# Kernel optimization log

Hardware: AMD Instinct MI355X
Metric: run time of the kernel (lower is better)

Reference implementation:

```python
import jax, jax.numpy as jnp
import numpy as np

N, E, G = 10000, 100000, 64
NB, EMB, S, COUT, LMAX = 16, 16, 8, 16, 2
RMAX = 4.0
WNUM = (LMAX + 1) * COUT * S * S  # 3072 per-edge TP weights


def setup_inputs() -> dict:
    key = jax.random.key(0)
    ks = jax.random.split(key, 16)
    def lin(k, i, o):
        return (jax.random.normal(k, (i, o), jnp.float32) / np.sqrt(i)).astype(jnp.float32)
    return {
        "pos": jax.random.normal(ks[0], (N, 3), jnp.float32),
        "A": jax.random.randint(ks[1], (N,), 0, 10),
        "batch": jnp.sort(jax.random.randint(ks[2], (N,), 0, G)),
        "edge_src": jax.random.randint(ks[3], (E,), 0, N),
        "edge_dst": jax.random.randint(ks[4], (E,), 0, N),
        "edge_shifts": jnp.zeros((E, 3), jnp.float32),
        "cell": jax.random.normal(ks[5], (G, 3, 3), jnp.float32),
        "emb_table": jax.random.normal(ks[6], (10, EMB), jnp.float32),
        "mlp_w1": lin(ks[7], EMB, 64), "mlp_b1": jnp.zeros((64,), jnp.float32),
        "mlp_w2": lin(ks[8], 64, S), "mlp_b2": jnp.zeros((S,), jnp.float32),
        "fc_w1": lin(ks[9], NB, 64), "fc_b1": jnp.zeros((64,), jnp.float32),
        "fc_w2": lin(ks[10], 64, 64), "fc_b2": jnp.zeros((64,), jnp.float32),
        "fc_w3": lin(ks[11], 64, WNUM), "fc_b3": jnp.zeros((WNUM,), jnp.float32),
    }


def _forward(pos, edge_shifts, cell, emb_table, mlp_w1, mlp_b1, mlp_w2, mlp_b2,
             fc_w1, fc_b1, fc_w2, fc_b2, fc_w3, fc_b3, A, batch, edge_src, edge_dst):
    # periodic-image edge vectors: shifts @ cell[graph of src node]
    shift = jnp.einsum('ei,eij->ej', edge_shifts, cell[batch[edge_src]])
    vec = pos[edge_dst] - pos[edge_src] + shift                     # (E,3)
    r = jnp.linalg.norm(vec, axis=1)                                # (E,)
    n = vec / jnp.maximum(r, 1e-9)[:, None]                         # unit edge direction
    # per-node scalar features: atom_mlp(atom_embedding(A))
    Ai = jax.nn.silu(emb_table[A] @ mlp_w1 + mlp_b1) @ mlp_w2 + mlp_b2  # (N,S)
    # radial basis: gaussian soft-one-hot on [0, RMAX] with cutoff, * sqrt(NB)
    vals = jnp.linspace(0.0, RMAX, NB + 2)[1:-1]
    step = RMAX / (NB + 1)
    emb = jnp.exp(-(((r[:, None] - vals) / step) ** 2)) / 1.12 * np.sqrt(NB)  # (E,NB)
    # radial MLP -> per-edge tensor-product weights
    h = jax.nn.silu(emb @ fc_w1 + fc_b1)
    h = jax.nn.silu(h @ fc_w2 + fc_b2)
    W = (h @ fc_w3 + fc_b3).reshape(E, LMAX + 1, COUT, S, S)        # (E,L,Cout,C1,C2)
    # f_in rank-L block is Ai[src] x n^{(x)L}; x2 is scalar Ai[dst].
    # The Cartesian TP factorizes: channel mixing once, then attach n^{(x)L}.
    fs, fd = Ai[edge_src], Ai[edge_dst]                             # (E,S)
    m = jnp.einsum('eloab,ea,eb->elo', W, fs, fd)                   # (E,L,Cout)
    out0 = m[:, 0]                                                  # (E,Cout)       rank 0
    out1 = m[:, 1, :, None] * n[:, None, :]                         # (E,Cout,3)     rank 1
    n2 = n[:, :, None] * n[:, None, :]                              # (E,3,3)
    out2 = m[:, 2, :, None, None] * n2[:, None]                     # (E,Cout,3,3)   rank 2
    ef = jnp.concatenate([out0, out1.reshape(E, -1), out2.reshape(E, -1)], axis=-1)  # (E, 13*Cout)
    # scatter-sum to destination nodes, normalize by neighbor count (clamped to 1)
    cnt = jnp.maximum(jax.ops.segment_sum(jnp.ones((E,), ef.dtype), edge_dst, num_segments=N), 1.0)
    return jax.ops.segment_sum(ef, edge_dst, num_segments=N) / cnt[:, None]  # (N, 208)


def reference(pos, A, batch, edge_src, edge_dst, edge_shifts, cell, emb_table,
              mlp_w1, mlp_b1, mlp_w2, mlp_b2, fc_w1, fc_b1, fc_w2, fc_b2, fc_w3, fc_b3):
    return _forward(pos, edge_shifts, cell, emb_table, mlp_w1, mlp_b1, mlp_w2, mlp_b2,
                    fc_w1, fc_b1, fc_w2, fc_b2, fc_w3, fc_b3, A, batch, edge_src, edge_dst)
```

## Files before the change

kernel.cpp:

```cpp
#include <hip/hip_runtime.h>
#include <math.h>
#include <stdint.h>


typedef float  f32x4  __attribute__((ext_vector_type(4)));
typedef short  s16x8  __attribute__((ext_vector_type(8)));
typedef __bf16 bf16x8 __attribute__((ext_vector_type(8)));

__device__ __forceinline__ float silu_f(float x) {
    return x / (1.0f + __expf(-x));
}

__device__ __forceinline__ void split8(f32x4 a, f32x4 b, s16x8& hi, s16x8& lo) {
    bf16x8 h8, l8;
    #pragma unroll
    for (int i = 0; i < 4; ++i) {
        float z = a[i]; __bf16 zh = (__bf16)z; h8[i] = zh; l8[i] = (__bf16)(z - (float)zh);
        float y = b[i]; __bf16 yh = (__bf16)y; h8[4 + i] = yh; l8[4 + i] = (__bf16)(y - (float)yh);
    }
    hi = __builtin_bit_cast(s16x8, h8);
    lo = __builtin_bit_cast(s16x8, l8);
}

__global__ __launch_bounds__(256) void k_setup(const float* __restrict__ w3,
                                               const float* __restrict__ b3,
                                               ushort* __restrict__ wz,
                                               const int* __restrict__ A,
                                               const float* __restrict__ embt,
                                               const float* __restrict__ w1,
                                               const float* __restrict__ b1,
                                               const float* __restrict__ w2,
                                               const float* __restrict__ b2,
                                               float* __restrict__ Ai,
                                               const int* __restrict__ edst,
                                               int* __restrict__ deg,
                                               int N, int E, int aiB) {
    const int b = blockIdx.x;
    const int tid = threadIdx.x;
    if (b < 780) {
        int t = b * 256 + tid;
        int j    = t & 7;
        int l    = (t >> 3) & 63;
        int rest = t >> 9;
        int tt   = rest % 3;
        int s    = rest / 3;
        int lo   = tt * 16 + (l & 15);
        int kl   = (l >> 4) * 8 + j;
        float v;
        if (s < 128) {
            int ab = s >> 1;
            int c  = (s & 1) * 32 + kl;
            v = w3[c * 3072 + lo * 64 + ab];
        } else {
            int ab = (s - 128) * 32 + kl;
            v = b3[lo * 64 + ab];
        }
        __bf16 hi  = (__bf16)v;
        __bf16 lor = (__bf16)(v - (float)hi);
        size_t base = (size_t)(s * 3 + tt) * 2 * 512 + l * 8 + j;
        wz[base]       = __builtin_bit_cast(ushort, hi);
        wz[base + 512] = __builtin_bit_cast(ushort, lor);
    } else if (b < 780 + aiB) {
        int i = (b - 780) * 256 + tid;
        if (i >= N) return;
        float e[16];
        const float* er = embt + A[i] * 16;
        #pragma unroll
        for (int k = 0; k < 16; ++k) e[k] = er[k];
        float h1[64];
        #pragma unroll
        for (int j = 0; j < 64; ++j) {
            float a = b1[j];
            #pragma unroll
            for (int k = 0; k < 16; ++k) a = fmaf(e[k], w1[k * 64 + j], a);
            h1[j] = silu_f(a);
        }
        #pragma unroll
        for (int o = 0; o < 8; ++o) {
            float a = b2[o];
            #pragma unroll
            for (int j = 0; j < 64; ++j) a = fmaf(h1[j], w2[j * 8 + o], a);
            Ai[i * 8 + o] = a;
        }
    } else {
        int e = (b - 780 - aiB) * 256 + tid;
        if (e < E) atomicAdd(&deg[edst[e]], 1);
    }
}

__global__ __launch_bounds__(1024) void k_scan(const int* __restrict__ deg,
                                               int* __restrict__ offs,
                                               int* __restrict__ cursor, int N) {
    __shared__ int part[1024];
    const int t = threadIdx.x;
    const int chunk = (N + 1023) / 1024;
    const int beg = t * chunk;
    const int end = min(beg + chunk, N);
    int s = 0;
    for (int i = beg; i < end; ++i) s += deg[i];
    part[t] = s;
    __syncthreads();
    for (int off = 1; off < 1024; off <<= 1) {
        int v = (t >= off) ? part[t - off] : 0;
        __syncthreads();
        part[t] += v;
        __syncthreads();
    }
    int run = (t == 0) ? 0 : part[t - 1];
    for (int i = beg; i < end; ++i) {
        offs[i] = run;
        cursor[i] = run;
        run += deg[i];
    }
    if (t == 1023) offs[N] = part[1023];
}

__global__ __launch_bounds__(256, 2) void k_edge(
    const float* __restrict__ pos, const int* __restrict__ batch,
    const int* __restrict__ esrc, const int* __restrict__ edst,
    const float* __restrict__ eshift, const float* __restrict__ cell,
    const float* __restrict__ fw1, const float* __restrict__ fb1,
    const float* __restrict__ fw2, const float* __restrict__ fb2,
    const ushort* __restrict__ wz,
    const float* __restrict__ Ai, float* __restrict__ ef,
    int* __restrict__ cursor, int* __restrict__ eidx, int E) {

    __shared__ __align__(16) float s_un[8704];
    __shared__ __align__(16) float s_o[8704];

    const int tid  = threadIdx.x;
    const int lane = tid & 63;
    const int w    = __builtin_amdgcn_readfirstlane(tid >> 6);
    const int e0   = blockIdx.x * 128;
    const int j0   = w * 16;

    const f32x4* wzv = reinterpret_cast<const f32x4*>(wz);
    f32x4 r0 = wzv[w * 192 + lane];
    f32x4 r1 = wzv[w * 192 + 64 + lane];
    f32x4 r2 = wzv[w * 192 + 128 + lane];

    #pragma unroll
    for (int rr = 0; rr < 2; ++rr) {
        const int e = e0 + rr * 64 + lane;
        const bool valid = (e < E);
        const int ec = valid ? e : (E - 1);
        const int src = esrc[ec];
        const int dst = edst[ec];

        const int g0 = batch[src];
        const float s0 = eshift[ec * 3 + 0], s1 = eshift[ec * 3 + 1], s2 = eshift[ec * 3 + 2];
        const float* cl = cell + g0 * 9;
        float vx = pos[dst * 3 + 0] - pos[src * 3 + 0] + s0 * cl[0] + s1 * cl[3] + s2 * cl[6];
        float vy = pos[dst * 3 + 1] - pos[src * 3 + 1] + s0 * cl[1] + s1 * cl[4] + s2 * cl[7];
        float vz = pos[dst * 3 + 2] - pos[src * 3 + 2] + s0 * cl[2] + s1 * cl[5] + s2 * cl[8];
        float r = sqrtf(vx * vx + vy * vy + vz * vz);
        float rinv = 1.0f / fmaxf(r, 1e-9f);
        float nx = vx * rinv, ny = vy * rinv, nz = vz * rinv;

        float embv[16];
        const float step = 4.0f / 17.0f;
        const float sc = 4.0f / 1.12f;
        #pragma unroll
        for (int k = 0; k < 16; ++k) {
            float d = (r - (float)(k + 1) * step) / step;
            embv[k] = __expf(-d * d) * sc;
        }

        const int hb = (rr * 64 + lane) * 65;
        #pragma unroll
        for (int jj = 0; jj < 16; ++jj) {
            const int j = j0 + jj;
            float a = fb1[j];
            #pragma unroll
            for (int k = 0; k < 16; ++k) a = fmaf(embv[k], fw1[k * 64 + j], a);
            s_un[hb + j] = silu_f(a);
        }

        {
            const float* As = Ai + (size_t)src * 8;
            const float* Ad = Ai + (size_t)dst * 8;
            float fsa0 = As[2 * w], fsa1 = As[2 * w + 1];
            f32x4 d0 = *reinterpret_cast<const f32x4*>(Ad);
            f32x4 d1 = *reinterpret_cast<const f32x4*>(Ad + 4);
            float fdv[8] = {d0[0], d0[1], d0[2], d0[3], d1[0], d1[1], d1[2], d1[3]};
            const int ob = (rr * 64 + lane) * 68 + j0;
            #pragma unroll
            for (int i = 0; i < 8; ++i)  s_o[ob + i]     = fsa0 * fdv[i];
            #pragma unroll
            for (int i = 0; i < 8; ++i)  s_o[ob + 8 + i] = fsa1 * fdv[i];
        }

        if (w == 0 && valid) {
            float* np = ef + (size_t)e * 52;
            np[48] = nx; np[49] = ny; np[50] = nz;
            int pp = atomicAdd(&cursor[dst], 1);
            eidx[pp] = e;
        }
    }
    __syncthreads();

    float hcr[2][16];
    #pragma unroll
    for (int rr = 0; rr < 2; ++rr) {
        const int hb = (rr * 64 + lane) * 65;
        #pragma unroll
        for (int i = 0; i < 16; ++i) hcr[rr][i] = fb2[j0 + i];
        #pragma unroll 4
        for (int j = 0; j < 64; ++j) {
            const float v = s_un[hb + j];
            const float* w2r = fw2 + j * 64 + j0;
            #pragma unroll
            for (int i = 0; i < 16; ++i) hcr[rr][i] = fmaf(v, w2r[i], hcr[rr][i]);
        }
        #pragma unroll
        for (int i = 0; i < 16; ++i) hcr[rr][i] = silu_f(hcr[rr][i]);
    }
    __syncthreads();

    #pragma unroll
    for (int rr = 0; rr < 2; ++rr) {
        const int hb = (rr * 64 + lane) * 68 + j0;
        #pragma unroll
        for (int i = 0; i < 16; ++i) s_un[hb + i] = hcr[rr][i];
    }
    __syncthreads();

    const int g = lane >> 4;
    const int mrow = w * 32 + (lane & 15);
    s16x8 AhF[2][2], AlF[2][2], OhF[2][2], OlF[2][2];
    #pragma unroll
    for (int mt = 0; mt < 2; ++mt) {
        const float* hr = s_un + (mrow + mt * 16) * 68;
        const float* orw = s_o + (mrow + mt * 16) * 68;
        f32x4 a0 = *reinterpret_cast<const f32x4*>(hr + g * 8);
        f32x4 a1 = *reinterpret_cast<const f32x4*>(hr + g * 8 + 4);
        split8(a0, a1, AhF[mt][0], AlF[mt][0]);
        f32x4 a2 = *reinterpret_cast<const f32x4*>(hr + 32 + g * 8);
        f32x4 a3 = *reinterpret_cast<const f32x4*>(hr + 32 + g * 8 + 4);
        split8(a2, a3, AhF[mt][1], AlF[mt][1]);
        f32x4 o0 = *reinterpret_cast<const f32x4*>(orw + g * 8);
        f32x4 o1 = *reinterpret_cast<const f32x4*>(orw + g * 8 + 4);
        split8(o0, o1, OhF[mt][0], OlF[mt][0]);
        f32x4 o2 = *reinterpret_cast<const f32x4*>(orw + 32 + g * 8);
        f32x4 o3 = *reinterpret_cast<const f32x4*>(orw + 32 + g * 8 + 4);
        split8(o2, o3, OhF[mt][1], OlF[mt][1]);
    }
    __syncthreads();

    ushort* sBb = reinterpret_cast<ushort*>(s_un);
    const int rb = w * 32 + (lane >> 4) * 4;

    f32x4 acc[2][3];
    #pragma unroll
    for (int mt = 0; mt < 2; ++mt)
        #pragma unroll
        for (int t = 0; t < 3; ++t) acc[mt][t] = (f32x4){0.f, 0.f, 0.f, 0.f};

    for (int u = 0; u < 65; ++u) {
        const int bs = u & 1;
        f32x4* db = reinterpret_cast<f32x4*>(sBb + bs * 6144 + w * 1536);
        db[lane]       = r0;
        db[64 + lane]  = r1;
        db[128 + lane] = r2;
        __syncthreads();
        if (u < 64) {
            const f32x4* gs = wzv + (size_t)(u + 1) * 768 + w * 192;
            r0 = gs[lane];
            r1 = gs[64 + lane];
            r2 = gs[128 + lane];
        }
        const ushort* bbuf = sBb + bs * 6144;
        if (u < 64) {
            float ov[8];
            #pragma unroll
            for (int i = 0; i < 4; ++i) {
                ov[i]     = s_o[(rb + i) * 68 + u];
                ov[4 + i] = s_o[(rb + 16 + i) * 68 + u];
            }
            #pragma unroll
            for (int t = 0; t < 3; ++t) {
                f32x4 D0 = {0.f, 0.f, 0.f, 0.f};
                f32x4 D1 = {0.f, 0.f, 0.f, 0.f};
                #pragma unroll
                for (int sl = 0; sl < 2; ++sl) {
                    const int fo = ((sl * 3 + t) * 2) * 512 + lane * 8;
                    s16x8 Bh = *reinterpret_cast<const s16x8*>(bbuf + fo);
                    s16x8 Bl = *reinterpret_cast<const s16x8*>(bbuf + fo + 512);
                    D0 = __builtin_amdgcn_mfma_f32_16x16x32_bf16(AhF[0][sl], Bh, D0, 0, 0, 0);
                    D0 = __builtin_amdgcn_mfma_f32_16x16x32_bf16(AhF[0][sl], Bl, D0, 0, 0, 0);
                    D0 = __builtin_amdgcn_mfma_f32_16x16x32_bf16(AlF[0][sl], Bh, D0, 0, 0, 0);
                    D1 = __builtin_amdgcn_mfma_f32_16x16x32_bf16(AhF[1][sl], Bh, D1, 0, 0, 0);
                    D1 = __builtin_amdgcn_mfma_f32_16x16x32_bf16(AhF[1][sl], Bl, D1, 0, 0, 0);
                    D1 = __builtin_amdgcn_mfma_f32_16x16x32_bf16(AlF[1][sl], Bh, D1, 0, 0, 0);
                }
                #pragma unroll
                for (int i = 0; i < 4; ++i) {
                    acc[0][t][i] = fmaf(ov[i],     D0[i], acc[0][t][i]);
                    acc[1][t][i] = fmaf(ov[4 + i], D1[i], acc[1][t][i]);
                }
            }
        } else {
            #pragma unroll
            for (int t = 0; t < 3; ++t) {
                #pragma unroll
                for (int sl = 0; sl < 2; ++sl) {
                    const int fo = ((sl * 3 + t) * 2) * 512 + lane * 8;
                    s16x8 Bh = *reinterpret_cast<const s16x8*>(bbuf + fo);
                    s16x8 Bl = *reinterpret_cast<const s16x8*>(bbuf + fo + 512);
                    acc[0][t] = __builtin_amdgcn_mfma_f32_16x16x32_bf16(OhF[0][sl], Bh, acc[0][t], 0, 0, 0);
                    acc[0][t] = __builtin_amdgcn_mfma_f32_16x16x32_bf16(OhF[0][sl], Bl, acc[0][t], 0, 0, 0);
                    acc[0][t] = __builtin_amdgcn_mfma_f32_16x16x32_bf16(OlF[0][sl], Bh, acc[0][t], 0, 0, 0);
                    acc[1][t] = __builtin_amdgcn_mfma_f32_16x16x32_bf16(OhF[1][sl], Bh, acc[1][t], 0, 0, 0);
                    acc[1][t] = __builtin_amdgcn_mfma_f32_16x16x32_bf16(OhF[1][sl], Bl, acc[1][t], 0, 0, 0);
                    acc[1][t] = __builtin_amdgcn_mfma_f32_16x16x32_bf16(OlF[1][sl], Bh, acc[1][t], 0, 0, 0);
                }
            }
        }
    }

    #pragma unroll
    for (int mt = 0; mt < 2; ++mt) {
        #pragma unroll
        for (int t = 0; t < 3; ++t) {
            #pragma unroll
            for (int i = 0; i < 4; ++i) {
                const int ee = e0 + rb + mt * 16 + i;
                if (ee < E) ef[(size_t)ee * 52 + t * 16 + (lane & 15)] = acc[mt][t][i];
            }
        }
    }
}

__global__ __launch_bounds__(256) void k_gather(const float* __restrict__ ef,
                                                const int* __restrict__ offs,
                                                const int* __restrict__ eidx,
                                                float* __restrict__ out, int N) {
    const int lane = threadIdx.x & 63;
    const int node = blockIdx.x * 4 + (threadIdx.x >> 6);
    if (node >= N) return;

    const int beg = offs[node];
    const int end = offs[node + 1];

    int mi[4], ii[4], jj[4], mode[4];
    #pragma unroll
    for (int t = 0; t < 4; ++t) {
        int c = lane + 64 * t;
        if (c < 16)       { mi[t] = c;                 ii[t] = 0;     jj[t] = 0;     mode[t] = 0; }
        else if (c < 64)  { int u = c - 16; mi[t] = 16 + u / 3; ii[t] = u % 3; jj[t] = 0; mode[t] = 1; }
        else if (c < 208) { int u = c - 64; mi[t] = 32 + u / 9; int rr = u % 9; ii[t] = rr / 3; jj[t] = rr % 3; mode[t] = 2; }
        else              { mi[t] = 0; ii[t] = 0; jj[t] = 0; mode[t] = 3; }
    }

    float acc[4] = {0.f, 0.f, 0.f, 0.f};
    for (int k = beg; k < end; ++k) {
        const int e = eidx[k];
        const float* b = ef + (size_t)e * 52;
        float v = (lane < 51) ? b[lane] : 0.0f;
        float n0 = __shfl(v, 48);
        float n1 = __shfl(v, 49);
        float n2 = __shfl(v, 50);
        #pragma unroll
        for (int t = 0; t < 4; ++t) {
            float mval = __shfl(v, mi[t]);
            float ni = (ii[t] == 0) ? n0 : ((ii[t] == 1) ? n1 : n2);
            float nj = (jj[t] == 0) ? n0 : ((jj[t] == 1) ? n1 : n2);
            float f  = (mode[t] == 0) ? 1.0f
                     : (mode[t] == 1) ? ni
                     : (mode[t] == 2) ? ni * nj
                     : 0.0f;
            acc[t] = fmaf(mval, f, acc[t]);
        }
    }

    const float inv = 1.0f / fmaxf((float)(end - beg), 1.0f);
    float* op = out + (size_t)node * 208;
    op[lane]        = acc[0] * inv;
    op[lane + 64]   = acc[1] * inv;
    op[lane + 128]  = acc[2] * inv;
    if (lane < 16) op[lane + 192] = acc[3] * inv;
}

extern "C" void kernel_launch(void* const* d_in, const int* in_sizes, int n_in,
                              void* d_out, int out_size, void* d_ws, size_t ws_size,
                              hipStream_t stream) {
    const float* pos    = (const float*)d_in[0];
    const int*   A      = (const int*)d_in[1];
    const int*   batch  = (const int*)d_in[2];
    const int*   esrc   = (const int*)d_in[3];
    const int*   edst   = (const int*)d_in[4];
    const float* eshift = (const float*)d_in[5];
    const float* cell   = (const float*)d_in[6];
    const float* embt   = (const float*)d_in[7];
    const float* mw1    = (const float*)d_in[8];
    const float* mb1    = (const float*)d_in[9];
    const float* mw2    = (const float*)d_in[10];
    const float* mb2    = (const float*)d_in[11];
    const float* fw1    = (const float*)d_in[12];
    const float* fb1    = (const float*)d_in[13];
    const float* fw2    = (const float*)d_in[14];
    const float* fb2    = (const float*)d_in[15];
    const float* w3     = (const float*)d_in[16];
    const float* b3     = (const float*)d_in[17];
    float* out = (float*)d_out;

    const int N = in_sizes[1];
    const int E = in_sizes[3];

    char* p = (char*)d_ws;
    auto take = [&](size_t bytes) {
        char* q = p;
        p += (bytes + 255) & ~(size_t)255;
        return q;
    };
    ushort* wz    = (ushort*)take((size_t)130 * 3 * 2 * 512 * sizeof(ushort));
    float* Ai     = (float*)take((size_t)N * 8 * sizeof(float));
    int*   deg    = (int*)  take((size_t)N * sizeof(int));
    int*   offs   = (int*)  take((size_t)(N + 1) * sizeof(int));
    int*   cursor = (int*)  take((size_t)N * sizeof(int));
    int*   eidx   = (int*)  take((size_t)E * sizeof(int));
    float* ef     = (float*)take((size_t)E * 52 * sizeof(float));

    hipMemsetAsync(deg, 0, (size_t)N * sizeof(int), stream);

    const int aiB = (N + 255) / 256;
    const int histB = (E + 255) / 256;
    k_setup<<<780 + aiB + histB, 256, 0, stream>>>(w3, b3, wz, A, embt, mw1, mb1,
                                                   mw2, mb2, Ai, edst, deg, N, E, aiB);
    k_scan<<<1, 1024, 0, stream>>>(deg, offs, cursor, N);
    k_edge<<<(E + 127) / 128, 256, 0, stream>>>(pos, batch, esrc, edst, eshift, cell,
                                                fw1, fb1, fw2, fb2, wz, Ai,
                                                ef, cursor, eidx, E);
    k_gather<<<(N + 3) / 4, 256, 0, stream>>>(ef, offs, eidx, out, N);
}
```

Measured before the change: 248.2 us.

## Load TP weight fragments directly into registers, dropping LDS staging and barriers

The per-step B-matrix weight fragments are now loaded from global memory straight into a double-buffered register array, replacing the shared-memory staging buffer and the per-iteration __syncthreads. The loop is unrolled by two so it alternates register buffers, prefetching step u+1 while computing step u. The final o-weighted term runs first, and s_setprio is raised around the MFMA groups. Each wave now loads all 12 fragments itself instead of splitting the load across four waves, which raises VGPR pressure and global/L2 traffic and may lower occupancy.

```diff
diff --git a/kernel.cpp b/kernel.cpp
--- a/kernel.cpp
+++ b/kernel.cpp
@@ -135,9 +135,14 @@
     const int j0   = w * 16;
 
     const f32x4* wzv = reinterpret_cast<const f32x4*>(wz);
-    f32x4 r0 = wzv[w * 192 + lane];
-    f32x4 r1 = wzv[w * 192 + 64 + lane];
-    f32x4 r2 = wzv[w * 192 + 128 + lane];
+
+    s16x8 Ba[12], Bb[12];
+#define LOADB(ARR, U) { \
+    const f32x4* gs = wzv + (size_t)(U) * 768 + lane; \
+    _Pragma("unroll") \
+    for (int f = 0; f < 12; ++f) ARR[f] = __builtin_bit_cast(s16x8, gs[f * 64]); }
+
+    LOADB(Ba, 0);
 
     #pragma unroll
     for (int rr = 0; rr < 2; ++rr) {
@@ -224,6 +229,8 @@
         for (int i = 0; i < 16; ++i) s_un[hb + i] = hcr[rr][i];
     }
     __syncthreads();
+
+    LOADB(Bb, 64);
 
     const int g = lane >> 4;
     const int mrow = w * 32 + (lane & 15);
@@ -245,9 +252,7 @@
         f32x4 o3 = *reinterpret_cast<const f32x4*>(orw + 32 + g * 8 + 4);
         split8(o2, o3, OhF[mt][1], OlF[mt][1]);
     }
-    __syncthreads();
-
-    ushort* sBb = reinterpret_cast<ushort*>(s_un);
+
     const int rb = w * 32 + (lane >> 4) * 4;
 
     f32x4 acc[2][3];
@@ -256,67 +261,64 @@
         #pragma unroll
         for (int t = 0; t < 3; ++t) acc[mt][t] = (f32x4){0.f, 0.f, 0.f, 0.f};
 
-    for (int u = 0; u < 65; ++u) {
-        const int bs = u & 1;
-        f32x4* db = reinterpret_cast<f32x4*>(sBb + bs * 6144 + w * 1536);
-        db[lane]       = r0;
-        db[64 + lane]  = r1;
-        db[128 + lane] = r2;
-        __syncthreads();
-        if (u < 64) {
-            const f32x4* gs = wzv + (size_t)(u + 1) * 768 + w * 192;
-            r0 = gs[lane];
-            r1 = gs[64 + lane];
-            r2 = gs[128 + lane];
-        }
-        const ushort* bbuf = sBb + bs * 6144;
-        if (u < 64) {
-            float ov[8];
-            #pragma unroll
-            for (int i = 0; i < 4; ++i) {
-                ov[i]     = s_o[(rb + i) * 68 + u];
-                ov[4 + i] = s_o[(rb + 16 + i) * 68 + u];
-            }
-            #pragma unroll
-            for (int t = 0; t < 3; ++t) {
-                f32x4 D0 = {0.f, 0.f, 0.f, 0.f};
-                f32x4 D1 = {0.f, 0.f, 0.f, 0.f};
-                #pragma unroll
-                for (int sl = 0; sl < 2; ++sl) {
-                    const int fo = ((sl * 3 + t) * 2) * 512 + lane * 8;
-                    s16x8 Bh = *reinterpret_cast<const s16x8*>(bbuf + fo);
-                    s16x8 Bl = *reinterpret_cast<const s16x8*>(bbuf + fo + 512);
-                    D0 = __builtin_amdgcn_mfma_f32_16x16x32_bf16(AhF[0][sl], Bh, D0, 0, 0, 0);
-                    D0 = __builtin_amdgcn_mfma_f32_16x16x32_bf16(AhF[0][sl], Bl, D0, 0, 0, 0);
-                    D0 = __builtin_amdgcn_mfma_f32_16x16x32_bf16(AlF[0][sl], Bh, D0, 0, 0, 0);
-                    D1 = __builtin_amdgcn_mfma_f32_16x16x32_bf16(AhF[1][sl], Bh, D1, 0, 0, 0);
-                    D1 = __builtin_amdgcn_mfma_f32_16x16x32_bf16(AhF[1][sl], Bl, D1, 0, 0, 0);
-                    D1 = __builtin_amdgcn_mfma_f32_16x16x32_bf16(AlF[1][sl], Bh, D1, 0, 0, 0);
-                }
-                #pragma unroll
-                for (int i = 0; i < 4; ++i) {
-                    acc[0][t][i] = fmaf(ov[i],     D0[i], acc[0][t][i]);
-                    acc[1][t][i] = fmaf(ov[4 + i], D1[i], acc[1][t][i]);
-                }
-            }
-        } else {
-            #pragma unroll
-            for (int t = 0; t < 3; ++t) {
-                #pragma unroll
-                for (int sl = 0; sl < 2; ++sl) {
-                    const int fo = ((sl * 3 + t) * 2) * 512 + lane * 8;
-                    s16x8 Bh = *reinterpret_cast<const s16x8*>(bbuf + fo);
-                    s16x8 Bl = *reinterpret_cast<const s16x8*>(bbuf + fo + 512);
-                    acc[0][t] = __builtin_amdgcn_mfma_f32_16x16x32_bf16(OhF[0][sl], Bh, acc[0][t], 0, 0, 0);
-                    acc[0][t] = __builtin_amdgcn_mfma_f32_16x16x32_bf16(OhF[0][sl], Bl, acc[0][t], 0, 0, 0);
-                    acc[0][t] = __builtin_amdgcn_mfma_f32_16x16x32_bf16(OlF[0][sl], Bh, acc[0][t], 0, 0, 0);
-                    acc[1][t] = __builtin_amdgcn_mfma_f32_16x16x32_bf16(OhF[1][sl], Bh, acc[1][t], 0, 0, 0);
-                    acc[1][t] = __builtin_amdgcn_mfma_f32_16x16x32_bf16(OhF[1][sl], Bl, acc[1][t], 0, 0, 0);
-                    acc[1][t] = __builtin_amdgcn_mfma_f32_16x16x32_bf16(OlF[1][sl], Bh, acc[1][t], 0, 0, 0);
-                }
-            }
-        }
-    }
+    __builtin_amdgcn_s_setprio(1);
+    #pragma unroll
+    for (int t = 0; t < 3; ++t) {
+        #pragma unroll
+        for (int sl = 0; sl < 2; ++sl) {
+            s16x8 Bh = Bb[(sl * 3 + t) * 2];
+            s16x8 Bl = Bb[(sl * 3 + t) * 2 + 1];
+            acc[0][t] = __builtin_amdgcn_mfma_f32_16x16x32_bf16(OhF[0][sl], Bh, acc[0][t], 0, 0, 0);
+            acc[0][t] = __builtin_amdgcn_mfma_f32_16x16x32_bf16(OhF[0][sl], Bl, acc[0][t], 0, 0, 0);
+            acc[0][t] = __builtin_amdgcn_mfma_f32_16x16x32_bf16(OlF[0][sl], Bh, acc[0][t], 0, 0, 0);
+            acc[1][t] = __builtin_amdgcn_mfma_f32_16x16x32_bf16(OhF[1][sl], Bh, acc[1][t], 0, 0, 0);
+            acc[1][t] = __builtin_amdgcn_mfma_f32_16x16x32_bf16(OhF[1][sl], Bl, acc[1][t], 0, 0, 0);
+            acc[1][t] = __builtin_amdgcn_mfma_f32_16x16x32_bf16(OlF[1][sl], Bh, acc[1][t], 0, 0, 0);
+        }
+    }
+    __builtin_amdgcn_s_setprio(0);
+
+#define MSTEP(BC, U) { \
+    float ov[8]; \
+    _Pragma("unroll") \
+    for (int i = 0; i < 4; ++i) { \
+        ov[i]     = s_o[(rb + i) * 68 + (U)]; \
+        ov[4 + i] = s_o[(rb + 16 + i) * 68 + (U)]; \
+    } \
+    __builtin_amdgcn_s_setprio(1); \
+    _Pragma("unroll") \
+    for (int t = 0; t < 3; ++t) { \
+        f32x4 D0 = {0.f, 0.f, 0.f, 0.f}; \
+        f32x4 D1 = {0.f, 0.f, 0.f, 0.f}; \
+        _Pragma("unroll") \
+        for (int sl = 0; sl < 2; ++sl) { \
+            s16x8 Bh = BC[(sl * 3 + t) * 2]; \
+            s16x8 Bl = BC[(sl * 3 + t) * 2 + 1]; \
+            D0 = __builtin_amdgcn_mfma_f32_16x16x32_bf16(AhF[0][sl], Bh, D0, 0, 0, 0); \
+            D0 = __builtin_amdgcn_mfma_f32_16x16x32_bf16(AhF[0][sl], Bl, D0, 0, 0, 0); \
+            D0 = __builtin_amdgcn_mfma_f32_16x16x32_bf16(AlF[0][sl], Bh, D0, 0, 0, 0); \
+            D1 = __builtin_amdgcn_mfma_f32_16x16x32_bf16(AhF[1][sl], Bh, D1, 0, 0, 0); \
+            D1 = __builtin_amdgcn_mfma_f32_16x16x32_bf16(AhF[1][sl], Bl, D1, 0, 0, 0); \
+            D1 = __builtin_amdgcn_mfma_f32_16x16x32_bf16(AlF[1][sl], Bh, D1, 0, 0, 0); \
+        } \
+        __builtin_amdgcn_s_setprio(0); \
+        _Pragma("unroll") \
+        for (int i = 0; i < 4; ++i) { \
+            acc[0][t][i] = fmaf(ov[i],     D0[i], acc[0][t][i]); \
+            acc[1][t][i] = fmaf(ov[4 + i], D1[i], acc[1][t][i]); \
+        } \
+        __builtin_amdgcn_s_setprio(1); \
+    } \
+    __builtin_amdgcn_s_setprio(0); }
+
+    for (int u = 0; u < 64; u += 2) {
+        LOADB(Bb, u + 1);
+        MSTEP(Ba, u);
+        if (u + 2 < 64) LOADB(Ba, u + 2);
+        MSTEP(Bb, u + 1);
+    }
+#undef MSTEP
+#undef LOADB
 
     #pragma unroll
     for (int mt = 0; mt < 2; ++mt) {
```

Measured after the change: 244.4 us. Within noise of the previous version (-1.5%).

## Stream TP weights via async global-to-LDS triple-buffer ring and shrink LDS

Applied to the files above, without the earlier changes.

The weight stream in the edge kernel now uses a three-slot LDS ring fed by direct global-to-LDS loads issued two steps ahead. This replaces the register staging and the per-step stores into LDS. The per-edge outer-product table is replaced by a compact 20-float fs/fd row per edge, and products are formed on the fly. The freed LDS allows three blocks per CU, and s_setprio brackets the MFMA bursts. The gather loop is also unrolled. The risks are register pressure from the higher occupancy target and correctness of the manual waitcnt and barrier sequencing.

```diff
diff --git a/kernel.cpp b/kernel.cpp
--- a/kernel.cpp
+++ b/kernel.cpp
@@ -115,7 +115,7 @@
     if (t == 1023) offs[N] = part[1023];
 }
 
-__global__ __launch_bounds__(256, 2) void k_edge(
+__global__ __launch_bounds__(256, 3) void k_edge(
     const float* __restrict__ pos, const int* __restrict__ batch,
     const int* __restrict__ esrc, const int* __restrict__ edst,
     const float* __restrict__ eshift, const float* __restrict__ cell,
@@ -125,19 +125,15 @@
     const float* __restrict__ Ai, float* __restrict__ ef,
     int* __restrict__ cursor, int* __restrict__ eidx, int E) {
 
-    __shared__ __align__(16) float s_un[8704];
-    __shared__ __align__(16) float s_o[8704];
+    __shared__ __align__(16) float s_uni[9216];
+    __shared__ __align__(16) float s_fsfd[128 * 20];
 
     const int tid  = threadIdx.x;
     const int lane = tid & 63;
     const int w    = __builtin_amdgcn_readfirstlane(tid >> 6);
     const int e0   = blockIdx.x * 128;
     const int j0   = w * 16;
-
-    const f32x4* wzv = reinterpret_cast<const f32x4*>(wz);
-    f32x4 r0 = wzv[w * 192 + lane];
-    f32x4 r1 = wzv[w * 192 + 64 + lane];
-    f32x4 r2 = wzv[w * 192 + 128 + lane];
+    const int g    = lane >> 4;
 
     #pragma unroll
     for (int rr = 0; rr < 2; ++rr) {
@@ -173,28 +169,23 @@
             float a = fb1[j];
             #pragma unroll
             for (int k = 0; k < 16; ++k) a = fmaf(embv[k], fw1[k * 64 + j], a);
-            s_un[hb + j] = silu_f(a);
-        }
-
-        {
+            s_uni[hb + j] = silu_f(a);
+        }
+
+        if (w == 0) {
             const float* As = Ai + (size_t)src * 8;
             const float* Ad = Ai + (size_t)dst * 8;
-            float fsa0 = As[2 * w], fsa1 = As[2 * w + 1];
-            f32x4 d0 = *reinterpret_cast<const f32x4*>(Ad);
-            f32x4 d1 = *reinterpret_cast<const f32x4*>(Ad + 4);
-            float fdv[8] = {d0[0], d0[1], d0[2], d0[3], d1[0], d1[1], d1[2], d1[3]};
-            const int ob = (rr * 64 + lane) * 68 + j0;
-            #pragma unroll
-            for (int i = 0; i < 8; ++i)  s_o[ob + i]     = fsa0 * fdv[i];
-            #pragma unroll
-            for (int i = 0; i < 8; ++i)  s_o[ob + 8 + i] = fsa1 * fdv[i];
-        }
-
-        if (w == 0 && valid) {
-            float* np = ef + (size_t)e * 52;
-            np[48] = nx; np[49] = ny; np[50] = nz;
-            int pp = atomicAdd(&cursor[dst], 1);
-            eidx[pp] = e;
+            float* fr = s_fsfd + (rr * 64 + lane) * 20;
+            *reinterpret_cast<f32x4*>(fr)      = *reinterpret_cast<const f32x4*>(As);
+            *reinterpret_cast<f32x4*>(fr + 4)  = *reinterpret_cast<const f32x4*>(As + 4);
+            *reinterpret_cast<f32x4*>(fr + 8)  = *reinterpret_cast<const f32x4*>(Ad);
+            *reinterpret_cast<f32x4*>(fr + 12) = *reinterpret_cast<const f32x4*>(Ad + 4);
+            if (valid) {
+                float* np = ef + (size_t)e * 52;
+                np[48] = nx; np[49] = ny; np[50] = nz;
+                int pp = atomicAdd(&cursor[dst], 1);
+                eidx[pp] = e;
+            }
         }
     }
     __syncthreads();
@@ -207,7 +198,7 @@
         for (int i = 0; i < 16; ++i) hcr[rr][i] = fb2[j0 + i];
         #pragma unroll 4
         for (int j = 0; j < 64; ++j) {
-            const float v = s_un[hb + j];
+            const float v = s_uni[hb + j];
             const float* w2r = fw2 + j * 64 + j0;
             #pragma unroll
             for (int i = 0; i < 16; ++i) hcr[rr][i] = fmaf(v, w2r[i], hcr[rr][i]);
@@ -221,33 +212,49 @@
     for (int rr = 0; rr < 2; ++rr) {
         const int hb = (rr * 64 + lane) * 68 + j0;
         #pragma unroll
-        for (int i = 0; i < 16; ++i) s_un[hb + i] = hcr[rr][i];
+        for (int i = 0; i < 16; ++i) s_uni[hb + i] = hcr[rr][i];
     }
     __syncthreads();
 
-    const int g = lane >> 4;
     const int mrow = w * 32 + (lane & 15);
     s16x8 AhF[2][2], AlF[2][2], OhF[2][2], OlF[2][2];
     #pragma unroll
     for (int mt = 0; mt < 2; ++mt) {
-        const float* hr = s_un + (mrow + mt * 16) * 68;
-        const float* orw = s_o + (mrow + mt * 16) * 68;
+        const float* hr = s_uni + (mrow + mt * 16) * 68;
         f32x4 a0 = *reinterpret_cast<const f32x4*>(hr + g * 8);
         f32x4 a1 = *reinterpret_cast<const f32x4*>(hr + g * 8 + 4);
         split8(a0, a1, AhF[mt][0], AlF[mt][0]);
         f32x4 a2 = *reinterpret_cast<const f32x4*>(hr + 32 + g * 8);
         f32x4 a3 = *reinterpret_cast<const f32x4*>(hr + 32 + g * 8 + 4);
         split8(a2, a3, AhF[mt][1], AlF[mt][1]);
-        f32x4 o0 = *reinterpret_cast<const f32x4*>(orw + g * 8);
-        f32x4 o1 = *reinterpret_cast<const f32x4*>(orw + g * 8 + 4);
-        split8(o0, o1, OhF[mt][0], OlF[mt][0]);
-        f32x4 o2 = *reinterpret_cast<const f32x4*>(orw + 32 + g * 8);
-        f32x4 o3 = *reinterpret_cast<const f32x4*>(orw + 32 + g * 8 + 4);
-        split8(o2, o3, OhF[mt][1], OlF[mt][1]);
-    }
-    __syncthreads();
-
-    ushort* sBb = reinterpret_cast<ushort*>(s_un);
+        const float* fr = s_fsfd + (mrow + mt * 16) * 20;
+        float fsg  = fr[g];
+        float fsg4 = fr[4 + g];
+        f32x4 fda = *reinterpret_cast<const f32x4*>(fr + 8);
+        f32x4 fdb = *reinterpret_cast<const f32x4*>(fr + 12);
+        split8(fsg * fda,  fsg * fdb,  OhF[mt][0], OlF[mt][0]);
+        split8(fsg4 * fda, fsg4 * fdb, OhF[mt][1], OlF[mt][1]);
+    }
+
+    asm volatile("s_waitcnt lgkmcnt(0)" ::: "memory");
+    __builtin_amdgcn_s_barrier();
+    __builtin_amdgcn_sched_barrier(0);
+
+    ushort* ring = reinterpret_cast<ushort*>(s_uni);
+
+#define ISSUE(U, S) { \
+    const ushort* gsrc = wz + (size_t)(U) * 6144 + (w * 3) * 512 + lane * 8; \
+    ushort* ldst = ring + (S) * 6144 + (w * 3) * 512; \
+    __builtin_amdgcn_global_load_lds(gsrc,        ldst,        16, 0, 0); \
+    __builtin_amdgcn_global_load_lds(gsrc + 512,  ldst + 512,  16, 0, 0); \
+    __builtin_amdgcn_global_load_lds(gsrc + 1024, ldst + 1024, 16, 0, 0); }
+
+    ISSUE(0, 0);
+    ISSUE(1, 1);
+    asm volatile("s_waitcnt vmcnt(3)" ::: "memory");
+    __builtin_amdgcn_s_barrier();
+    __builtin_amdgcn_sched_barrier(0);
+
     const int rb = w * 32 + (lane >> 4) * 4;
 
     f32x4 acc[2][3];
@@ -256,27 +263,33 @@
         #pragma unroll
         for (int t = 0; t < 3; ++t) acc[mt][t] = (f32x4){0.f, 0.f, 0.f, 0.f};
 
-    for (int u = 0; u < 65; ++u) {
-        const int bs = u & 1;
-        f32x4* db = reinterpret_cast<f32x4*>(sBb + bs * 6144 + w * 1536);
-        db[lane]       = r0;
-        db[64 + lane]  = r1;
-        db[128 + lane] = r2;
-        __syncthreads();
+    float fs8[8];
+    int cur = 0;
+    for (int u = 0; u <= 64; ++u) {
+        if (u < 63) {
+            int s2 = cur + 2; if (s2 >= 3) s2 -= 3;
+            ISSUE(u + 2, s2);
+        }
+        const ushort* BB = ring + cur * 6144;
         if (u < 64) {
-            const f32x4* gs = wzv + (size_t)(u + 1) * 768 + w * 192;
-            r0 = gs[lane];
-            r1 = gs[64 + lane];
-            r2 = gs[128 + lane];
-        }
-        const ushort* bbuf = sBb + bs * 6144;
-        if (u < 64) {
+            if ((u & 7) == 0) {
+                const int q = u >> 3;
+                #pragma unroll
+                for (int i = 0; i < 4; ++i) {
+                    fs8[i]     = s_fsfd[(rb + i) * 20 + q];
+                    fs8[4 + i] = s_fsfd[(rb + 16 + i) * 20 + q];
+                }
+            }
             float ov[8];
-            #pragma unroll
-            for (int i = 0; i < 4; ++i) {
-                ov[i]     = s_o[(rb + i) * 68 + u];
-                ov[4 + i] = s_o[(rb + 16 + i) * 68 + u];
-            }
+            {
+                const int q = 8 + (u & 7);
+                #pragma unroll
+                for (int i = 0; i < 4; ++i) {
+                    ov[i]     = fs8[i]     * s_fsfd[(rb + i) * 20 + q];
+                    ov[4 + i] = fs8[4 + i] * s_fsfd[(rb + 16 + i) * 20 + q];
+                }
+            }
+            __builtin_amdgcn_s_setprio(1);
             #pragma unroll
             for (int t = 0; t < 3; ++t) {
                 f32x4 D0 = {0.f, 0.f, 0.f, 0.f};
@@ -284,8 +297,8 @@
                 #pragma unroll
                 for (int sl = 0; sl < 2; ++sl) {
                     const int fo = ((sl * 3 + t) * 2) * 512 + lane * 8;
-                    s16x8 Bh = *reinterpret_cast<const s16x8*>(bbuf + fo);
-                    s16x8 Bl = *reinterpret_cast<const s16x8*>(bbuf + fo + 512);
+                    s16x8 Bh = *reinterpret_cast<const s16x8*>(BB + fo);
+                    s16x8 Bl = *reinterpret_cast<const s16x8*>(BB + fo + 512);
                     D0 = __builtin_amdgcn_mfma_f32_16x16x32_bf16(AhF[0][sl], Bh, D0, 0, 0, 0);
                     D0 = __builtin_amdgcn_mfma_f32_16x16x32_bf16(AhF[0][sl], Bl, D0, 0, 0, 0);
                     D0 = __builtin_amdgcn_mfma_f32_16x16x32_bf16(AlF[0][sl], Bh, D0, 0, 0, 0);
@@ -293,20 +306,24 @@
                     D1 = __builtin_amdgcn_mfma_f32_16x16x32_bf16(AhF[1][sl], Bl, D1, 0, 0, 0);
                     D1 = __builtin_amdgcn_mfma_f32_16x16x32_bf16(AlF[1][sl], Bh, D1, 0, 0, 0);
                 }
+                __builtin_amdgcn_s_setprio(0);
                 #pragma unroll
                 for (int i = 0; i < 4; ++i) {
                     acc[0][t][i] = fmaf(ov[i],     D0[i], acc[0][t][i]);
                     acc[1][t][i] = fmaf(ov[4 + i], D1[i], acc[1][t][i]);
                 }
-            }
+                __builtin_amdgcn_s_setprio(1);
+            }
+            __builtin_amdgcn_s_setprio(0);
         } else {
+            __builtin_amdgcn_s_setprio(1);
             #pragma unroll
             for (int t = 0; t < 3; ++t) {
                 #pragma unroll
                 for (int sl = 0; sl < 2; ++sl) {
                     const int fo = ((sl * 3 + t) * 2) * 512 + lane * 8;
-                    s16x8 Bh = *reinterpret_cast<const s16x8*>(bbuf + fo);
-                    s16x8 Bl = *reinterpret_cast<const s16x8*>(bbuf + fo + 512);
+                    s16x8 Bh = *reinterpret_cast<const s16x8*>(BB + fo);
+                    s16x8 Bl = *reinterpret_cast<const s16x8*>(BB + fo + 512);
                     acc[0][t] = __builtin_amdgcn_mfma_f32_16x16x32_bf16(OhF[0][sl], Bh, acc[0][t], 0, 0, 0);
                     acc[0][t] = __builtin_amdgcn_mfma_f32_16x16x32_bf16(OhF[0][sl], Bl, acc[0][t], 0, 0, 0);
                     acc[0][t] = __builtin_amdgcn_mfma_f32_16x16x32_bf16(OlF[0][sl], Bh, acc[0][t], 0, 0, 0);
@@ -315,8 +332,20 @@
                     acc[1][t] = __builtin_amdgcn_mfma_f32_16x16x32_bf16(OlF[1][sl], Bh, acc[1][t], 0, 0, 0);
                 }
             }
-        }
-    }
+            __builtin_amdgcn_s_setprio(0);
+        }
+        if (u < 63) {
+            asm volatile("s_waitcnt vmcnt(3) lgkmcnt(0)" ::: "memory");
+            __builtin_amdgcn_s_barrier();
+            __builtin_amdgcn_sched_barrier(0);
+        } else if (u < 64) {
+            asm volatile("s_waitcnt vmcnt(0) lgkmcnt(0)" ::: "memory");
+            __builtin_amdgcn_s_barrier();
+            __builtin_amdgcn_sched_barrier(0);
+        }
+        cur = (cur == 2) ? 0 : cur + 1;
+    }
+#undef ISSUE
 
     #pragma unroll
     for (int mt = 0; mt < 2; ++mt) {
@@ -353,6 +382,7 @@
     }
 
     float acc[4] = {0.f, 0.f, 0.f, 0.f};
+    #pragma unroll 4
     for (int k = beg; k < end; ++k) {
         const int e = eidx[k];
         const float* b = ef + (size_t)e * 52;
```

Result: slower. 272.0 us (+9.6%).
